# Optimization experiments

Hardware: AMD Instinct MI355X
Metric: run time of the kernel (lower is better)

Reference implementation:

```python
import jax, jax.numpy as jnp
import numpy as np

N = 8192
PT_DIM = 3
ENC_DIM = 384
RADIUS = 0.12
ALPHA = 6.0
SQRT_D = ENC_DIM ** 0.5


def setup_inputs() -> dict:
    key = jax.random.key(0)
    k1, k2 = jax.random.split(key)
    pts = jax.random.uniform(k1, (N, PT_DIM), dtype=jnp.float32)  # points in unit cube
    # A corresponds to the (frozen) random-feature matrix: stacked standard normals * alpha
    A = jax.random.normal(k2, (PT_DIM, ENC_DIM), dtype=jnp.float32) * ALPHA
    return {"pts": pts, "A": A}


def reference(pts, A):
    # Radius-ball adjacency: J[i,j] = 1 if ||pts[i]-pts[j]|| < r (dist^2 < r^2, dist >= 0)
    d2 = jnp.sum((pts[:, None, :] - pts[None, :, :]) ** 2, axis=-1)  # (N, N)
    J = (d2 < RADIUS * RADIUS).astype(pts.dtype)                      # (N, N)

    pA = (pts / RADIUS) @ A            # (N, ENC_DIM)
    c, s = jnp.cos(pA), jnp.sin(pA)    # epA = [cos(pA), sin(pA)]

    # Neighbor aggregation: G = J @ epA, done per real/imag part
    Gr = J @ c                          # (N, ENC_DIM)
    Gi = J @ s

    # Complex phase division: (Gr + i Gi) / (cos + i sin)
    G = jax.lax.complex(Gr, Gi) / jax.lax.complex(c, s)

    # Row-wise normalization to norm sqrt(enc_dim)
    G = G / jnp.linalg.norm(G, axis=-1, keepdims=True) * SQRT_D
    return G
```

## Files before the change

kernel.cpp:

```cpp
#include <hip/hip_runtime.h>
#include <hip/hip_fp16.h>
#include <math.h>

#define N_PTS   8192
#define ENC     384
#define NTHREAD 384
#define NCELL1  8
#define NCELLS  512
#define RADIUS  0.12f
#define MAXSUB  12
#define MAXU    352

__device__ __forceinline__ void fast_sincos(float x, float& s, float& c) {
    float rev = x * 0.15915494309189535f;
    rev -= rintf(rev);
    s = __builtin_amdgcn_sinf(rev);
    c = __builtin_amdgcn_cosf(rev);
}

__device__ __forceinline__ int cell_of(float x) {
    int c = (int)(x * 8.0f);
    return min(NCELL1 - 1, max(0, c));
}

static __device__ __forceinline__ unsigned h2u(__half2 h) { union { __half2 h; unsigned u; } x; x.h = h; return x.u; }
static __device__ __forceinline__ __half2 u2h(unsigned u) { union { unsigned u; __half2 h; } x; x.u = u; return x.h; }

static const size_t OFF_CSTART_I = 0;
static const size_t OFF_SPTS_B   = 520 * 4;
static const size_t OFF_CS_B     = OFF_SPTS_B + (size_t)N_PTS * 16;
static const size_t WS_FULL_B    = OFF_CS_B + (size_t)(N_PTS + 1) * ENC * 4 + 1024;

__global__ __launch_bounds__(1024) void k_prep(const float* __restrict__ pts,
                                               int* __restrict__ cell_start_g,
                                               float4* __restrict__ spts) {
    __shared__ int cnt[NCELLS];
    __shared__ int sc[NCELLS];
    __shared__ int cur[NCELLS];
    const int t = threadIdx.x;
    if (t < NCELLS) cnt[t] = 0;
    __syncthreads();

    int   cids[8];
    float xs[8], ys[8], zs[8];
    #pragma unroll
    for (int k = 0; k < 8; ++k) {
        int i = t + k * 1024;
        float x = pts[3 * i + 0], y = pts[3 * i + 1], z = pts[3 * i + 2];
        xs[k] = x; ys[k] = y; zs[k] = z;
        int cid = (cell_of(x) << 6) | (cell_of(y) << 3) | cell_of(z);
        cids[k] = cid;
        atomicAdd(&cnt[cid], 1);
    }
    __syncthreads();
    if (t < NCELLS) sc[t] = cnt[t];
    __syncthreads();
    for (int off = 1; off < NCELLS; off <<= 1) {
        int v = 0;
        if (t < NCELLS && t >= off) v = sc[t - off];
        __syncthreads();
        if (t < NCELLS) sc[t] += v;
        __syncthreads();
    }
    if (t < NCELLS) {
        int excl = sc[t] - cnt[t];
        cell_start_g[t] = excl;
        cur[t] = excl;
    }
    if (t == 0) cell_start_g[NCELLS] = N_PTS;
    __syncthreads();
    #pragma unroll
    for (int k = 0; k < 8; ++k) {
        int i = t + k * 1024;
        int pos = atomicAdd(&cur[cids[k]], 1);
        spts[pos] = make_float4(xs[k], ys[k], zs[k], __int_as_float(i));
    }
}

__global__ __launch_bounds__(NTHREAD) void k_encode(const float4* __restrict__ spts,
                                                    const float* __restrict__ A,
                                                    __half2* __restrict__ cs) {
    const int t  = threadIdx.x;
    const int p0 = blockIdx.x * 8;
    const float a0 = A[t], a1 = A[ENC + t], a2 = A[2 * ENC + t];
    #pragma unroll
    for (int k = 0; k < 8; ++k) {
        int p = p0 + k;
        if (p > N_PTS) break;
        if (p == N_PTS) {
            cs[(size_t)p * ENC + t] = __floats2half2_rn(0.f, 0.f);
            break;
        }
        float4 P = spts[p];
        float qx = __fdiv_rn(P.x, RADIUS);
        float qy = __fdiv_rn(P.y, RADIUS);
        float qz = __fdiv_rn(P.z, RADIUS);
        float pa = fmaf(qz, a2, fmaf(qy, a1, qx * a0));
        float s, c;
        fast_sincos(pa, s, c);
        cs[(size_t)p * ENC + t] = __floats2half2_rn(c, s);
    }
}

__global__ __launch_bounds__(NTHREAD) void k_main(const float4* __restrict__ spts,
                                                  const int* __restrict__ cell_start,
                                                  const uint4* __restrict__ cs4,
                                                  float* __restrict__ out, int out_mode) {
    const int b    = blockIdx.x;
    const int cell = (b & 7) * 64 + ((b >> 3) & 63);
    const int s    = b >> 9;
    const int t = threadIdx.x, lane = t & 63, wv = t >> 6;
    const int g = t / 96, q = t - g * 96;

    __shared__ int    run_lo[9], run_hi[9];
    __shared__ float4 own_l[4];
    __shared__ int    ne;
    __shared__ __align__(16) unsigned int ent_g[4][96];
    __shared__ uint4  comb_a[4][96];
    __shared__ uint4  comb_b[4][96];
    __shared__ float  red2[4][96];
    __shared__ float  scale_l[4];

    const int o_lo = cell_start[cell];
    const int o_hi = cell_start[cell + 1];
    const int n_own = o_hi - o_lo;
    if (n_own <= 0 || 4 * s >= n_own) return;

    const int cx = cell >> 6, cy = (cell >> 3) & 7, cz = cell & 7;
    if (t < 9) {
        int dx = t / 3 - 1, dy = t % 3 - 1;
        int cxx = cx + dx, cyy = cy + dy;
        int lo = 0, hi = 0;
        if (cxx >= 0 && cxx <= 7 && cyy >= 0 && cyy <= 7) {
            int basec = (cxx * 8 + cyy) * 8;
            int zlo = max(cz - 1, 0), zhi = min(cz + 1, 7);
            lo = cell_start[basec + zlo];
            hi = cell_start[basec + zhi + 1];
        }
        run_lo[t] = lo; run_hi[t] = hi;
    }

    const double R2 = (double)0.12 * (double)0.12;
    const float R2_LO = 0.0144f - 1e-6f;
    const float R2_HI = 0.0144f + 1e-6f;
    const uint4* csq = cs4 + q;

    for (int chunk = s; 4 * chunk < n_own; chunk += MAXSUB) {
        const int pbase = o_lo + 4 * chunk;
        const int np = min(4, o_hi - pbase);

        __syncthreads();
        if (t == 0) ne = 0;
        if (t < 4) {
            int idx = pbase + t;
            own_l[t] = (idx < o_hi) ? spts[idx] : make_float4(1e9f, 1e9f, 1e9f, 0.f);
        }
        __syncthreads();
        const float4 O0 = own_l[0], O1 = own_l[1], O2 = own_l[2], O3 = own_l[3];

        for (int r = wv; r < 9; r += 6) {
            const int lo = run_lo[r], hi = run_hi[r];
            for (int jb = lo; jb < hi; jb += 64) {
                int j = jb + lane;
                unsigned mk = 0;
                if (j < hi) {
                    float4 Pj = spts[j];
                    #define TEST(O, BIT) { \
                        float fdx = Pj.x - O.x, fdy = Pj.y - O.y, fdz = Pj.z - O.z; \
                        float d2f = fmaf(fdx, fdx, fmaf(fdy, fdy, fdz * fdz)); \
                        if (d2f < R2_LO) mk |= (BIT); \
                        else if (d2f <= R2_HI) { \
                            double ddx = (double)Pj.x - (double)O.x; \
                            double ddy = (double)Pj.y - (double)O.y; \
                            double ddz = (double)Pj.z - (double)O.z; \
                            if (ddx * ddx + ddy * ddy + ddz * ddz < R2) mk |= (BIT); \
                        } }
                    TEST(O0, 1u) TEST(O1, 2u) TEST(O2, 4u) TEST(O3, 8u)
                    #undef TEST
                }
                unsigned long long mask = __ballot(mk != 0);
                if (mask) {
                    int leader = __ffsll((long long)mask) - 1;
                    int basep = 0;
                    if (lane == leader) basep = atomicAdd(&ne, __popcll(mask));
                    basep = __shfl(basep, leader);
                    if (mk != 0) {
                        int pos = basep + __popcll(mask & ((1ull << lane) - 1ull));
                        if (pos < MAXU) ent_g[pos & 3][pos >> 2] = (unsigned)j | (mk << 16);
                    }
                }
            }
        }
        __syncthreads();
        const int ne_p  = min(ne, MAXU);
        const int total = (ne_p + 15) & ~15;
        if (t < total + 16 - ne_p) {
            int pos = ne_p + t;
            ent_g[pos & 3][pos >> 2] = (unsigned)N_PTS;
        }
        __syncthreads();
        const int P = total >> 2;

        __half2 ax0[4], ax1[4], ax2[4], ax3[4];
        #pragma unroll
        for (int dd = 0; dd < 4; ++dd) {
            ax0[dd] = u2h(0u); ax1[dd] = u2h(0u); ax2[dd] = u2h(0u); ax3[dd] = u2h(0u);
        }
        uint4 ev = *(const uint4*)&ent_g[g][0];
        uint4 r0 = csq[(size_t)(ev.x & 0xFFFFu) * 96];
        uint4 r1 = csq[(size_t)(ev.y & 0xFFFFu) * 96];
        uint4 r2 = csq[(size_t)(ev.z & 0xFFFFu) * 96];
        uint4 r3 = csq[(size_t)(ev.w & 0xFFFFu) * 96];
        for (int m = 0; m < P; m += 4) {
            uint4 ev_n = *(const uint4*)&ent_g[g][m + 4];
            uint4 n0 = csq[(size_t)(ev_n.x & 0xFFFFu) * 96];
            uint4 n1 = csq[(size_t)(ev_n.y & 0xFFFFu) * 96];
            uint4 n2 = csq[(size_t)(ev_n.z & 0xFFFFu) * 96];
            uint4 n3 = csq[(size_t)(ev_n.w & 0xFFFFu) * 96];
            #define ACC4(R, MK) { \
                unsigned mk_ = (MK); \
                __half2 h0 = u2h((mk_ & 1u) ? 0x3C003C00u : 0u); \
                __half2 h1 = u2h((mk_ & 2u) ? 0x3C003C00u : 0u); \
                __half2 h2 = u2h((mk_ & 4u) ? 0x3C003C00u : 0u); \
                __half2 h3 = u2h((mk_ & 8u) ? 0x3C003C00u : 0u); \
                __half2 rx = u2h(R.x), ry = u2h(R.y), rz = u2h(R.z), rw = u2h(R.w); \
                ax0[0] = __hfma2(rx, h0, ax0[0]); ax0[1] = __hfma2(ry, h0, ax0[1]); \
                ax0[2] = __hfma2(rz, h0, ax0[2]); ax0[3] = __hfma2(rw, h0, ax0[3]); \
                ax1[0] = __hfma2(rx, h1, ax1[0]); ax1[1] = __hfma2(ry, h1, ax1[1]); \
                ax1[2] = __hfma2(rz, h1, ax1[2]); ax1[3] = __hfma2(rw, h1, ax1[3]); \
                ax2[0] = __hfma2(rx, h2, ax2[0]); ax2[1] = __hfma2(ry, h2, ax2[1]); \
                ax2[2] = __hfma2(rz, h2, ax2[2]); ax2[3] = __hfma2(rw, h2, ax2[3]); \
                ax3[0] = __hfma2(rx, h3, ax3[0]); ax3[1] = __hfma2(ry, h3, ax3[1]); \
                ax3[2] = __hfma2(rz, h3, ax3[2]); ax3[3] = __hfma2(rw, h3, ax3[3]); }
            ACC4(r0, ev.x >> 16) ACC4(r1, ev.y >> 16) ACC4(r2, ev.z >> 16) ACC4(r3, ev.w >> 16)
            #undef ACC4
            ev = ev_n; r0 = n0; r1 = n1; r2 = n2; r3 = n3;
        }

        #define PACK4(A) make_uint4(h2u(A[0]), h2u(A[1]), h2u(A[2]), h2u(A[3]))
        #define ADDU(A, V) { A[0] = __hadd2(A[0], u2h(V.x)); A[1] = __hadd2(A[1], u2h(V.y)); \
                             A[2] = __hadd2(A[2], u2h(V.z)); A[3] = __hadd2(A[3], u2h(V.w)); }
        if (g == 1) { comb_a[0][q] = PACK4(ax0); comb_a[1][q] = PACK4(ax1);
                      comb_a[2][q] = PACK4(ax2); comb_a[3][q] = PACK4(ax3); }
        else if (g == 3) { comb_b[0][q] = PACK4(ax0); comb_b[1][q] = PACK4(ax1);
                           comb_b[2][q] = PACK4(ax2); comb_b[3][q] = PACK4(ax3); }
        __syncthreads();
        if (g == 0) { uint4 v0 = comb_a[0][q], v1 = comb_a[1][q], v2 = comb_a[2][q], v3 = comb_a[3][q];
                      ADDU(ax0, v0) ADDU(ax1, v1) ADDU(ax2, v2) ADDU(ax3, v3) }
        else if (g == 2) { uint4 v0 = comb_b[0][q], v1 = comb_b[1][q], v2 = comb_b[2][q], v3 = comb_b[3][q];
                           ADDU(ax0, v0) ADDU(ax1, v1) ADDU(ax2, v2) ADDU(ax3, v3) }
        __syncthreads();
        if (g == 2) { comb_a[0][q] = PACK4(ax0); comb_a[1][q] = PACK4(ax1);
                      comb_a[2][q] = PACK4(ax2); comb_a[3][q] = PACK4(ax3); }
        __syncthreads();
        if (g == 0) {
            uint4 v0 = comb_a[0][q], v1 = comb_a[1][q], v2 = comb_a[2][q], v3 = comb_a[3][q];
            ADDU(ax0, v0) ADDU(ax1, v1) ADDU(ax2, v2) ADDU(ax3, v3)
            #define NORM_P(AC, PP) { float m2 = 0.f; \
                _Pragma("unroll") for (int dd = 0; dd < 4; ++dd) { \
                    float2 f = __half22float2(AC[dd]); \
                    m2 = fmaf(f.x, f.x, fmaf(f.y, f.y, m2)); } \
                red2[PP][q] = m2; }
            NORM_P(ax0, 0) NORM_P(ax1, 1) NORM_P(ax2, 2) NORM_P(ax3, 3)
            #undef NORM_P
        }
        #undef PACK4
        #undef ADDU
        __syncthreads();
        if (t < 256) {
            int w = t >> 6, l = t & 63;
            float v = red2[w][l] + (l < 32 ? red2[w][64 + l] : 0.f);
            #pragma unroll
            for (int off = 32; off > 0; off >>= 1) v += __shfl_down(v, off);
            if (l == 0) scale_l[w] = sqrtf(384.0f / v);
        }
        __syncthreads();
        if (g == 0) {
            #define STORE_P(AC, PP) if ((PP) < np) { \
                const float scl = scale_l[PP]; \
                uint4 ov = csq[(size_t)(pbase + (PP)) * 96]; \
                float2 o0 = __half22float2(u2h(ov.x)), o1 = __half22float2(u2h(ov.y)); \
                float2 o2 = __half22float2(u2h(ov.z)), o3 = __half22float2(u2h(ov.w)); \
                float2 g0v = __half22float2(AC[0]), g1v = __half22float2(AC[1]); \
                float2 g2v = __half22float2(AC[2]), g3v = __half22float2(AC[3]); \
                float re0 = (g0v.x * o0.x + g0v.y * o0.y) * scl, im0 = (g0v.y * o0.x - g0v.x * o0.y) * scl; \
                float re1 = (g1v.x * o1.x + g1v.y * o1.y) * scl, im1 = (g1v.y * o1.x - g1v.x * o1.y) * scl; \
                float re2 = (g2v.x * o2.x + g2v.y * o2.y) * scl, im2 = (g2v.y * o2.x - g2v.x * o2.y) * scl; \
                float re3 = (g3v.x * o3.x + g3v.y * o3.y) * scl, im3 = (g3v.y * o3.x - g3v.x * o3.y) * scl; \
                const int o = __float_as_int(own_l[PP].w); \
                if (out_mode == 0) { \
                    ((float4*)out)[(size_t)o * 96 + q] = make_float4(re0, re1, re2, re3); \
                } else { \
                    ((float4*)out)[(size_t)o * 192 + 2 * q + 0] = make_float4(re0, im0, re1, im1); \
                    ((float4*)out)[(size_t)o * 192 + 2 * q + 1] = make_float4(re2, im2, re3, im3); \
                } }
            STORE_P(ax0, 0) STORE_P(ax1, 1) STORE_P(ax2, 2) STORE_P(ax3, 3)
            #undef STORE_P
        }
    }
}

__global__ __launch_bounds__(NTHREAD) void vecKM_allpairs(const float* __restrict__ pts,
                                                          const float* __restrict__ A,
                                                          float* __restrict__ out, int out_mode) {
    const int i = blockIdx.x;
    const int t = threadIdx.x;
    __shared__ float nb_x[512], nb_y[512], nb_z[512];
    __shared__ int nb_cnt;
    __shared__ float red[8];
    if (t == 0) nb_cnt = 0;
    __syncthreads();
    const float xi = pts[3 * i + 0], yi = pts[3 * i + 1], zi = pts[3 * i + 2];
    const double dxi = xi, dyi = yi, dzi = zi;
    const double R2 = (double)0.12 * (double)0.12;
    const float R2_LO = 0.0144f - 1e-6f, R2_HI = 0.0144f + 1e-6f;
    const int lane = t & 63;
    for (int jb = 0; jb < N_PTS; jb += NTHREAD) {
        const int j = jb + t;
        bool isnb = false;
        float xj = 0.f, yj = 0.f, zj = 0.f;
        if (j < N_PTS) {
            xj = pts[3 * j + 0]; yj = pts[3 * j + 1]; zj = pts[3 * j + 2];
            float fdx = xj - xi, fdy = yj - yi, fdz = zj - zi;
            float d2f = fmaf(fdx, fdx, fmaf(fdy, fdy, fdz * fdz));
            if (d2f < R2_LO) isnb = true;
            else if (d2f <= R2_HI) {
                double dx = (double)xj - dxi, dy = (double)yj - dyi, dz = (double)zj - dzi;
                isnb = (dx * dx + dy * dy + dz * dz) < R2;
            }
        }
        unsigned long long mask = __ballot(isnb);
        if (mask) {
            int leader = __ffsll((long long)mask) - 1;
            int basep = 0;
            if (lane == leader) basep = atomicAdd(&nb_cnt, __popcll(mask));
            basep = __shfl(basep, leader);
            if (isnb) {
                int pos = basep + __popcll(mask & ((1ull << lane) - 1ull));
                if (pos < 512) {
                    nb_x[pos] = (xj - xi) * (1.0f / 0.12f);
                    nb_y[pos] = (yj - yi) * (1.0f / 0.12f);
                    nb_z[pos] = (zj - zi) * (1.0f / 0.12f);
                }
            }
        }
    }
    __syncthreads();
    const int nn = min(nb_cnt, 512);
    const float a0 = A[t], a1 = A[ENC + t], a2 = A[2 * ENC + t];
    float gr = 0.f, gi = 0.f;
    #pragma unroll 4
    for (int m = 0; m < nn; ++m) {
        float pa = fmaf(nb_z[m], a2, fmaf(nb_y[m], a1, nb_x[m] * a0));
        float sv, cv;
        fast_sincos(pa, sv, cv);
        gr += cv; gi += sv;
    }
    float m2 = fmaf(gr, gr, gi * gi);
    #pragma unroll
    for (int off = 32; off > 0; off >>= 1) m2 += __shfl_down(m2, off);
    const int wid = t >> 6;
    if (lane == 0) red[wid] = m2;
    __syncthreads();
    if (t == 0) {
        float tot = 0.f;
        for (int w = 0; w < NTHREAD / 64; ++w) tot += red[w];
        red[7] = tot;
    }
    __syncthreads();
    const float scale = sqrtf(384.0f / red[7]);
    const float re = gr * scale, im = gi * scale;
    if (out_mode == 0) out[i * ENC + t] = re;
    else ((float2*)out)[i * ENC + t] = make_float2(re, im);
}

extern "C" void kernel_launch(void* const* d_in, const int* in_sizes, int n_in,
                              void* d_out, int out_size, void* d_ws, size_t ws_size,
                              hipStream_t stream) {
    const float* pts = (const float*)d_in[0];
    const float* A   = (const float*)d_in[1];
    float* out = (float*)d_out;
    const int out_mode = (out_size >= 2 * N_PTS * ENC) ? 1 : 0;

    if (ws_size >= WS_FULL_B) {
        int*     cell_start = (int*)d_ws + OFF_CSTART_I;
        float4*  spts       = (float4*)((char*)d_ws + OFF_SPTS_B);
        __half2* cs         = (__half2*)((char*)d_ws + OFF_CS_B);

        k_prep<<<1, 1024, 0, stream>>>(pts, cell_start, spts);
        k_encode<<<(N_PTS / 8) + 1, NTHREAD, 0, stream>>>(spts, A, cs);
        k_main<<<8 * 64 * MAXSUB, NTHREAD, 0, stream>>>(spts, cell_start,
                                                        (const uint4*)cs, out, out_mode);
    } else {
        vecKM_allpairs<<<N_PTS, NTHREAD, 0, stream>>>(pts, A, out, out_mode);
    }
}
```

Measured before the change: 73.77 us.

## Split point binning into multi-block kernels and schedule k_main via chunk descriptors

The single-block preprocessing kernel is replaced by a memset plus separate count, scan and scatter kernels, so binning runs across 16 blocks instead of one 1024-thread block. The scan also builds a descriptor table mapping each k_main block to one (cell, 4-point chunk), so each block handles exactly one chunk instead of looping over chunks with a fixed stride of 12. The software prefetch of the next neighbor entries in the accumulation loop is removed, and MAXU grows slightly. This adds more kernel launches and drops the per-slab chunk capacity to 384, which silently skips chunks if a slab overflows.

```diff
diff --git a/kernel.cpp b/kernel.cpp
--- a/kernel.cpp
+++ b/kernel.cpp
@@ -8,8 +8,9 @@
 #define NCELL1  8
 #define NCELLS  512
 #define RADIUS  0.12f
-#define MAXSUB  12
-#define MAXU    352
+#define MAXU    368
+#define NCH_SLAB 384
+#define GRID_MAIN (8 * NCH_SLAB)
 
 __device__ __forceinline__ void fast_sincos(float x, float& s, float& c) {
     float rev = x * 0.15915494309189535f;
@@ -26,55 +27,77 @@
 static __device__ __forceinline__ unsigned h2u(__half2 h) { union { __half2 h; unsigned u; } x; x.h = h; return x.u; }
 static __device__ __forceinline__ __half2 u2h(unsigned u) { union { unsigned u; __half2 h; } x; x.u = u; return x.h; }
 
-static const size_t OFF_CSTART_I = 0;
-static const size_t OFF_SPTS_B   = 520 * 4;
-static const size_t OFF_CS_B     = OFF_SPTS_B + (size_t)N_PTS * 16;
-static const size_t WS_FULL_B    = OFF_CS_B + (size_t)(N_PTS + 1) * ENC * 4 + 1024;
-
-__global__ __launch_bounds__(1024) void k_prep(const float* __restrict__ pts,
-                                               int* __restrict__ cell_start_g,
-                                               float4* __restrict__ spts) {
-    __shared__ int cnt[NCELLS];
-    __shared__ int sc[NCELLS];
-    __shared__ int cur[NCELLS];
+static const size_t OFF_CNT_I    = 0;
+static const size_t OFF_CSTART_I = 512;
+static const size_t OFF_CURSOR_I = 1032;
+static const size_t OFF_CELLID_I = 1544;
+static const size_t OFF_DESC_I   = 9736;
+static const size_t INT_END_B    = 12808u * 4;
+static const size_t OFF_SPTS_B   = INT_END_B;
+static const size_t OFF_CS_B     = OFF_SPTS_B + 131072;
+static const size_t WS_FULL_B    = OFF_CS_B + (size_t)(N_PTS + 1) * ENC * 4;
+
+__global__ __launch_bounds__(512) void k_count(const float* __restrict__ pts,
+                                               int* __restrict__ cnt,
+                                               int* __restrict__ cell_id) {
+    int i = blockIdx.x * 512 + threadIdx.x;
+    if (i >= N_PTS) return;
+    int cid = (cell_of(pts[3 * i + 0]) << 6) | (cell_of(pts[3 * i + 1]) << 3)
+            | cell_of(pts[3 * i + 2]);
+    cell_id[i] = cid;
+    atomicAdd(&cnt[cid], 1);
+}
+
+__global__ __launch_bounds__(512) void k_scan(const int* __restrict__ cnt,
+                                              int* __restrict__ cell_start,
+                                              int* __restrict__ cursor,
+                                              int* __restrict__ desc) {
+    __shared__ int sc[512];
+    __shared__ int sch[512];
     const int t = threadIdx.x;
-    if (t < NCELLS) cnt[t] = 0;
-    __syncthreads();
-
-    int   cids[8];
-    float xs[8], ys[8], zs[8];
-    #pragma unroll
-    for (int k = 0; k < 8; ++k) {
-        int i = t + k * 1024;
-        float x = pts[3 * i + 0], y = pts[3 * i + 1], z = pts[3 * i + 2];
-        xs[k] = x; ys[k] = y; zs[k] = z;
-        int cid = (cell_of(x) << 6) | (cell_of(y) << 3) | cell_of(z);
-        cids[k] = cid;
-        atomicAdd(&cnt[cid], 1);
-    }
-    __syncthreads();
-    if (t < NCELLS) sc[t] = cnt[t];
-    __syncthreads();
-    for (int off = 1; off < NCELLS; off <<= 1) {
-        int v = 0;
-        if (t < NCELLS && t >= off) v = sc[t - off];
+    const int c = cnt[t];
+
+    sc[t] = c;
+    __syncthreads();
+    for (int off = 1; off < 512; off <<= 1) {
+        int v = (t >= off) ? sc[t - off] : 0;
         __syncthreads();
-        if (t < NCELLS) sc[t] += v;
+        sc[t] += v;
         __syncthreads();
     }
-    if (t < NCELLS) {
-        int excl = sc[t] - cnt[t];
-        cell_start_g[t] = excl;
-        cur[t] = excl;
-    }
-    if (t == 0) cell_start_g[NCELLS] = N_PTS;
-    __syncthreads();
-    #pragma unroll
-    for (int k = 0; k < 8; ++k) {
-        int i = t + k * 1024;
-        int pos = atomicAdd(&cur[cids[k]], 1);
-        spts[pos] = make_float4(xs[k], ys[k], zs[k], __int_as_float(i));
-    }
+    cell_start[t] = sc[t] - c;
+    cursor[t]     = sc[t] - c;
+    if (t == 511) cell_start[NCELLS] = sc[511];
+
+    const int nch = (c + 3) >> 2;
+    sch[t] = nch;
+    __syncthreads();
+    for (int off = 1; off < 64; off <<= 1) {
+        int v = ((t & 63) >= off) ? sch[t - off] : 0;
+        __syncthreads();
+        sch[t] += v;
+        __syncthreads();
+    }
+    const int rank = sch[t] - nch;
+
+    for (int i = t; i < GRID_MAIN; i += 512) desc[i] = -1;
+    __syncthreads();
+    const int slab = t >> 6;
+    for (int k = 0; k < nch; ++k) {
+        int pos = rank + k;
+        if (pos < NCH_SLAB) desc[slab + 8 * pos] = (t << 6) | k;
+    }
+}
+
+__global__ __launch_bounds__(512) void k_scatter(const float* __restrict__ pts,
+                                                 const int* __restrict__ cell_id,
+                                                 int* __restrict__ cursor,
+                                                 float4* __restrict__ spts) {
+    int i = blockIdx.x * 512 + threadIdx.x;
+    if (i >= N_PTS) return;
+    int pos = atomicAdd(&cursor[cell_id[i]], 1);
+    spts[pos] = make_float4(pts[3 * i + 0], pts[3 * i + 1], pts[3 * i + 2],
+                            __int_as_float(i));
 }
 
 __global__ __launch_bounds__(NTHREAD) void k_encode(const float4* __restrict__ spts,
@@ -104,11 +127,13 @@
 
 __global__ __launch_bounds__(NTHREAD) void k_main(const float4* __restrict__ spts,
                                                   const int* __restrict__ cell_start,
+                                                  const int* __restrict__ desc_g,
                                                   const uint4* __restrict__ cs4,
                                                   float* __restrict__ out, int out_mode) {
-    const int b    = blockIdx.x;
-    const int cell = (b & 7) * 64 + ((b >> 3) & 63);
-    const int s    = b >> 9;
+    const int d = desc_g[blockIdx.x];
+    if (d < 0) return;
+    const int cell = d >> 6;
+    const int kk   = d & 63;
     const int t = threadIdx.x, lane = t & 63, wv = t >> 6;
     const int g = t / 96, q = t - g * 96;
 
@@ -123,8 +148,8 @@
 
     const int o_lo = cell_start[cell];
     const int o_hi = cell_start[cell + 1];
-    const int n_own = o_hi - o_lo;
-    if (n_own <= 0 || 4 * s >= n_own) return;
+    const int pbase = o_lo + (kk << 2);
+    const int np = min(4, o_hi - pbase);
 
     const int cx = cell >> 6, cy = (cell >> 3) & 7, cz = cell & 7;
     if (t < 9) {
@@ -139,164 +164,151 @@
         }
         run_lo[t] = lo; run_hi[t] = hi;
     }
+    if (t == 0) ne = 0;
+    if (t < 4) {
+        int idx = pbase + t;
+        own_l[t] = (idx < o_hi) ? spts[idx] : make_float4(1e9f, 1e9f, 1e9f, 0.f);
+    }
+    __syncthreads();
+    const float4 O0 = own_l[0], O1 = own_l[1], O2 = own_l[2], O3 = own_l[3];
 
     const double R2 = (double)0.12 * (double)0.12;
     const float R2_LO = 0.0144f - 1e-6f;
     const float R2_HI = 0.0144f + 1e-6f;
     const uint4* csq = cs4 + q;
 
-    for (int chunk = s; 4 * chunk < n_own; chunk += MAXSUB) {
-        const int pbase = o_lo + 4 * chunk;
-        const int np = min(4, o_hi - pbase);
-
-        __syncthreads();
-        if (t == 0) ne = 0;
-        if (t < 4) {
-            int idx = pbase + t;
-            own_l[t] = (idx < o_hi) ? spts[idx] : make_float4(1e9f, 1e9f, 1e9f, 0.f);
-        }
-        __syncthreads();
-        const float4 O0 = own_l[0], O1 = own_l[1], O2 = own_l[2], O3 = own_l[3];
-
-        for (int r = wv; r < 9; r += 6) {
-            const int lo = run_lo[r], hi = run_hi[r];
-            for (int jb = lo; jb < hi; jb += 64) {
-                int j = jb + lane;
-                unsigned mk = 0;
-                if (j < hi) {
-                    float4 Pj = spts[j];
-                    #define TEST(O, BIT) { \
-                        float fdx = Pj.x - O.x, fdy = Pj.y - O.y, fdz = Pj.z - O.z; \
-                        float d2f = fmaf(fdx, fdx, fmaf(fdy, fdy, fdz * fdz)); \
-                        if (d2f < R2_LO) mk |= (BIT); \
-                        else if (d2f <= R2_HI) { \
-                            double ddx = (double)Pj.x - (double)O.x; \
-                            double ddy = (double)Pj.y - (double)O.y; \
-                            double ddz = (double)Pj.z - (double)O.z; \
-                            if (ddx * ddx + ddy * ddy + ddz * ddz < R2) mk |= (BIT); \
-                        } }
-                    TEST(O0, 1u) TEST(O1, 2u) TEST(O2, 4u) TEST(O3, 8u)
-                    #undef TEST
-                }
-                unsigned long long mask = __ballot(mk != 0);
-                if (mask) {
-                    int leader = __ffsll((long long)mask) - 1;
-                    int basep = 0;
-                    if (lane == leader) basep = atomicAdd(&ne, __popcll(mask));
-                    basep = __shfl(basep, leader);
-                    if (mk != 0) {
-                        int pos = basep + __popcll(mask & ((1ull << lane) - 1ull));
-                        if (pos < MAXU) ent_g[pos & 3][pos >> 2] = (unsigned)j | (mk << 16);
-                    }
+    for (int r = wv; r < 9; r += 6) {
+        const int lo = run_lo[r], hi = run_hi[r];
+        for (int jb = lo; jb < hi; jb += 64) {
+            int j = jb + lane;
+            unsigned mk = 0;
+            if (j < hi) {
+                float4 Pj = spts[j];
+                #define TEST(O, BIT) { \
+                    float fdx = Pj.x - O.x, fdy = Pj.y - O.y, fdz = Pj.z - O.z; \
+                    float d2f = fmaf(fdx, fdx, fmaf(fdy, fdy, fdz * fdz)); \
+                    if (d2f < R2_LO) mk |= (BIT); \
+                    else if (d2f <= R2_HI) { \
+                        double ddx = (double)Pj.x - (double)O.x; \
+                        double ddy = (double)Pj.y - (double)O.y; \
+                        double ddz = (double)Pj.z - (double)O.z; \
+                        if (ddx * ddx + ddy * ddy + ddz * ddz < R2) mk |= (BIT); \
+                    } }
+                TEST(O0, 1u) TEST(O1, 2u) TEST(O2, 4u) TEST(O3, 8u)
+                #undef TEST
+            }
+            unsigned long long mask = __ballot(mk != 0);
+            if (mask) {
+                int leader = __ffsll((long long)mask) - 1;
+                int basep = 0;
+                if (lane == leader) basep = atomicAdd(&ne, __popcll(mask));
+                basep = __shfl(basep, leader);
+                if (mk != 0) {
+                    int pos = basep + __popcll(mask & ((1ull << lane) - 1ull));
+                    if (pos < MAXU) ent_g[pos & 3][pos >> 2] = (unsigned)j | (mk << 16);
                 }
             }
         }
-        __syncthreads();
-        const int ne_p  = min(ne, MAXU);
-        const int total = (ne_p + 15) & ~15;
-        if (t < total + 16 - ne_p) {
-            int pos = ne_p + t;
-            ent_g[pos & 3][pos >> 2] = (unsigned)N_PTS;
-        }
-        __syncthreads();
-        const int P = total >> 2;
-
-        __half2 ax0[4], ax1[4], ax2[4], ax3[4];
-        #pragma unroll
-        for (int dd = 0; dd < 4; ++dd) {
-            ax0[dd] = u2h(0u); ax1[dd] = u2h(0u); ax2[dd] = u2h(0u); ax3[dd] = u2h(0u);
-        }
-        uint4 ev = *(const uint4*)&ent_g[g][0];
+    }
+    __syncthreads();
+    const int ne_p  = min(ne, MAXU);
+    const int total = (ne_p + 15) & ~15;
+    if (t < total - ne_p) {
+        int pos = ne_p + t;
+        ent_g[pos & 3][pos >> 2] = (unsigned)N_PTS;
+    }
+    __syncthreads();
+    const int P = total >> 2;
+
+    __half2 ax0[4], ax1[4], ax2[4], ax3[4];
+    #pragma unroll
+    for (int dd = 0; dd < 4; ++dd) {
+        ax0[dd] = u2h(0u); ax1[dd] = u2h(0u); ax2[dd] = u2h(0u); ax3[dd] = u2h(0u);
+    }
+    for (int m = 0; m < P; m += 4) {
+        uint4 ev = *(const uint4*)&ent_g[g][m];
         uint4 r0 = csq[(size_t)(ev.x & 0xFFFFu) * 96];
         uint4 r1 = csq[(size_t)(ev.y & 0xFFFFu) * 96];
         uint4 r2 = csq[(size_t)(ev.z & 0xFFFFu) * 96];
         uint4 r3 = csq[(size_t)(ev.w & 0xFFFFu) * 96];
-        for (int m = 0; m < P; m += 4) {
-            uint4 ev_n = *(const uint4*)&ent_g[g][m + 4];
-            uint4 n0 = csq[(size_t)(ev_n.x & 0xFFFFu) * 96];
-            uint4 n1 = csq[(size_t)(ev_n.y & 0xFFFFu) * 96];
-            uint4 n2 = csq[(size_t)(ev_n.z & 0xFFFFu) * 96];
-            uint4 n3 = csq[(size_t)(ev_n.w & 0xFFFFu) * 96];
-            #define ACC4(R, MK) { \
-                unsigned mk_ = (MK); \
-                __half2 h0 = u2h((mk_ & 1u) ? 0x3C003C00u : 0u); \
-                __half2 h1 = u2h((mk_ & 2u) ? 0x3C003C00u : 0u); \
-                __half2 h2 = u2h((mk_ & 4u) ? 0x3C003C00u : 0u); \
-                __half2 h3 = u2h((mk_ & 8u) ? 0x3C003C00u : 0u); \
-                __half2 rx = u2h(R.x), ry = u2h(R.y), rz = u2h(R.z), rw = u2h(R.w); \
-                ax0[0] = __hfma2(rx, h0, ax0[0]); ax0[1] = __hfma2(ry, h0, ax0[1]); \
-                ax0[2] = __hfma2(rz, h0, ax0[2]); ax0[3] = __hfma2(rw, h0, ax0[3]); \
-                ax1[0] = __hfma2(rx, h1, ax1[0]); ax1[1] = __hfma2(ry, h1, ax1[1]); \
-                ax1[2] = __hfma2(rz, h1, ax1[2]); ax1[3] = __hfma2(rw, h1, ax1[3]); \
-                ax2[0] = __hfma2(rx, h2, ax2[0]); ax2[1] = __hfma2(ry, h2, ax2[1]); \
-                ax2[2] = __hfma2(rz, h2, ax2[2]); ax2[3] = __hfma2(rw, h2, ax2[3]); \
-                ax3[0] = __hfma2(rx, h3, ax3[0]); ax3[1] = __hfma2(ry, h3, ax3[1]); \
-                ax3[2] = __hfma2(rz, h3, ax3[2]); ax3[3] = __hfma2(rw, h3, ax3[3]); }
-            ACC4(r0, ev.x >> 16) ACC4(r1, ev.y >> 16) ACC4(r2, ev.z >> 16) ACC4(r3, ev.w >> 16)
-            #undef ACC4
-            ev = ev_n; r0 = n0; r1 = n1; r2 = n2; r3 = n3;
-        }
-
-        #define PACK4(A) make_uint4(h2u(A[0]), h2u(A[1]), h2u(A[2]), h2u(A[3]))
-        #define ADDU(A, V) { A[0] = __hadd2(A[0], u2h(V.x)); A[1] = __hadd2(A[1], u2h(V.y)); \
-                             A[2] = __hadd2(A[2], u2h(V.z)); A[3] = __hadd2(A[3], u2h(V.w)); }
-        if (g == 1) { comb_a[0][q] = PACK4(ax0); comb_a[1][q] = PACK4(ax1);
-                      comb_a[2][q] = PACK4(ax2); comb_a[3][q] = PACK4(ax3); }
-        else if (g == 3) { comb_b[0][q] = PACK4(ax0); comb_b[1][q] = PACK4(ax1);
-                           comb_b[2][q] = PACK4(ax2); comb_b[3][q] = PACK4(ax3); }
-        __syncthreads();
-        if (g == 0) { uint4 v0 = comb_a[0][q], v1 = comb_a[1][q], v2 = comb_a[2][q], v3 = comb_a[3][q];
-                      ADDU(ax0, v0) ADDU(ax1, v1) ADDU(ax2, v2) ADDU(ax3, v3) }
-        else if (g == 2) { uint4 v0 = comb_b[0][q], v1 = comb_b[1][q], v2 = comb_b[2][q], v3 = comb_b[3][q];
-                           ADDU(ax0, v0) ADDU(ax1, v1) ADDU(ax2, v2) ADDU(ax3, v3) }
-        __syncthreads();
-        if (g == 2) { comb_a[0][q] = PACK4(ax0); comb_a[1][q] = PACK4(ax1);
-                      comb_a[2][q] = PACK4(ax2); comb_a[3][q] = PACK4(ax3); }
-        __syncthreads();
-        if (g == 0) {
-            uint4 v0 = comb_a[0][q], v1 = comb_a[1][q], v2 = comb_a[2][q], v3 = comb_a[3][q];
-            ADDU(ax0, v0) ADDU(ax1, v1) ADDU(ax2, v2) ADDU(ax3, v3)
-            #define NORM_P(AC, PP) { float m2 = 0.f; \
-                _Pragma("unroll") for (int dd = 0; dd < 4; ++dd) { \
-                    float2 f = __half22float2(AC[dd]); \
-                    m2 = fmaf(f.x, f.x, fmaf(f.y, f.y, m2)); } \
-                red2[PP][q] = m2; }
-            NORM_P(ax0, 0) NORM_P(ax1, 1) NORM_P(ax2, 2) NORM_P(ax3, 3)
-            #undef NORM_P
-        }
-        #undef PACK4
-        #undef ADDU
-        __syncthreads();
-        if (t < 256) {
-            int w = t >> 6, l = t & 63;
-            float v = red2[w][l] + (l < 32 ? red2[w][64 + l] : 0.f);
-            #pragma unroll
-            for (int off = 32; off > 0; off >>= 1) v += __shfl_down(v, off);
-            if (l == 0) scale_l[w] = sqrtf(384.0f / v);
-        }
-        __syncthreads();
-        if (g == 0) {
-            #define STORE_P(AC, PP) if ((PP) < np) { \
-                const float scl = scale_l[PP]; \
-                uint4 ov = csq[(size_t)(pbase + (PP)) * 96]; \
-                float2 o0 = __half22float2(u2h(ov.x)), o1 = __half22float2(u2h(ov.y)); \
-                float2 o2 = __half22float2(u2h(ov.z)), o3 = __half22float2(u2h(ov.w)); \
-                float2 g0v = __half22float2(AC[0]), g1v = __half22float2(AC[1]); \
-                float2 g2v = __half22float2(AC[2]), g3v = __half22float2(AC[3]); \
-                float re0 = (g0v.x * o0.x + g0v.y * o0.y) * scl, im0 = (g0v.y * o0.x - g0v.x * o0.y) * scl; \
-                float re1 = (g1v.x * o1.x + g1v.y * o1.y) * scl, im1 = (g1v.y * o1.x - g1v.x * o1.y) * scl; \
-                float re2 = (g2v.x * o2.x + g2v.y * o2.y) * scl, im2 = (g2v.y * o2.x - g2v.x * o2.y) * scl; \
-                float re3 = (g3v.x * o3.x + g3v.y * o3.y) * scl, im3 = (g3v.y * o3.x - g3v.x * o3.y) * scl; \
-                const int o = __float_as_int(own_l[PP].w); \
-                if (out_mode == 0) { \
-                    ((float4*)out)[(size_t)o * 96 + q] = make_float4(re0, re1, re2, re3); \
-                } else { \
-                    ((float4*)out)[(size_t)o * 192 + 2 * q + 0] = make_float4(re0, im0, re1, im1); \
-                    ((float4*)out)[(size_t)o * 192 + 2 * q + 1] = make_float4(re2, im2, re3, im3); \
-                } }
-            STORE_P(ax0, 0) STORE_P(ax1, 1) STORE_P(ax2, 2) STORE_P(ax3, 3)
-            #undef STORE_P
-        }
+        #define ACC4(R, MK) { \
+            unsigned mk_ = (MK); \
+            __half2 h0 = u2h((mk_ & 1u) ? 0x3C003C00u : 0u); \
+            __half2 h1 = u2h((mk_ & 2u) ? 0x3C003C00u : 0u); \
+            __half2 h2 = u2h((mk_ & 4u) ? 0x3C003C00u : 0u); \
+            __half2 h3 = u2h((mk_ & 8u) ? 0x3C003C00u : 0u); \
+            __half2 rx = u2h(R.x), ry = u2h(R.y), rz = u2h(R.z), rw = u2h(R.w); \
+            ax0[0] = __hfma2(rx, h0, ax0[0]); ax0[1] = __hfma2(ry, h0, ax0[1]); \
+            ax0[2] = __hfma2(rz, h0, ax0[2]); ax0[3] = __hfma2(rw, h0, ax0[3]); \
+            ax1[0] = __hfma2(rx, h1, ax1[0]); ax1[1] = __hfma2(ry, h1, ax1[1]); \
+            ax1[2] = __hfma2(rz, h1, ax1[2]); ax1[3] = __hfma2(rw, h1, ax1[3]); \
+            ax2[0] = __hfma2(rx, h2, ax2[0]); ax2[1] = __hfma2(ry, h2, ax2[1]); \
+            ax2[2] = __hfma2(rz, h2, ax2[2]); ax2[3] = __hfma2(rw, h2, ax2[3]); \
+            ax3[0] = __hfma2(rx, h3, ax3[0]); ax3[1] = __hfma2(ry, h3, ax3[1]); \
+            ax3[2] = __hfma2(rz, h3, ax3[2]); ax3[3] = __hfma2(rw, h3, ax3[3]); }
+        ACC4(r0, ev.x >> 16) ACC4(r1, ev.y >> 16) ACC4(r2, ev.z >> 16) ACC4(r3, ev.w >> 16)
+        #undef ACC4
+    }
+
+    #define PACK4(A) make_uint4(h2u(A[0]), h2u(A[1]), h2u(A[2]), h2u(A[3]))
+    #define ADDU(A, V) { A[0] = __hadd2(A[0], u2h(V.x)); A[1] = __hadd2(A[1], u2h(V.y)); \
+                         A[2] = __hadd2(A[2], u2h(V.z)); A[3] = __hadd2(A[3], u2h(V.w)); }
+    if (g == 1) { comb_a[0][q] = PACK4(ax0); comb_a[1][q] = PACK4(ax1);
+                  comb_a[2][q] = PACK4(ax2); comb_a[3][q] = PACK4(ax3); }
+    else if (g == 3) { comb_b[0][q] = PACK4(ax0); comb_b[1][q] = PACK4(ax1);
+                       comb_b[2][q] = PACK4(ax2); comb_b[3][q] = PACK4(ax3); }
+    __syncthreads();
+    if (g == 0) { uint4 v0 = comb_a[0][q], v1 = comb_a[1][q], v2 = comb_a[2][q], v3 = comb_a[3][q];
+                  ADDU(ax0, v0) ADDU(ax1, v1) ADDU(ax2, v2) ADDU(ax3, v3) }
+    else if (g == 2) { uint4 v0 = comb_b[0][q], v1 = comb_b[1][q], v2 = comb_b[2][q], v3 = comb_b[3][q];
+                       ADDU(ax0, v0) ADDU(ax1, v1) ADDU(ax2, v2) ADDU(ax3, v3) }
+    __syncthreads();
+    if (g == 2) { comb_a[0][q] = PACK4(ax0); comb_a[1][q] = PACK4(ax1);
+                  comb_a[2][q] = PACK4(ax2); comb_a[3][q] = PACK4(ax3); }
+    __syncthreads();
+    if (g == 0) {
+        uint4 v0 = comb_a[0][q], v1 = comb_a[1][q], v2 = comb_a[2][q], v3 = comb_a[3][q];
+        ADDU(ax0, v0) ADDU(ax1, v1) ADDU(ax2, v2) ADDU(ax3, v3)
+        #define NORM_P(AC, PP) { float m2 = 0.f; \
+            _Pragma("unroll") for (int dd = 0; dd < 4; ++dd) { \
+                float2 f = __half22float2(AC[dd]); \
+                m2 = fmaf(f.x, f.x, fmaf(f.y, f.y, m2)); } \
+            red2[PP][q] = m2; }
+        NORM_P(ax0, 0) NORM_P(ax1, 1) NORM_P(ax2, 2) NORM_P(ax3, 3)
+        #undef NORM_P
+    }
+    #undef PACK4
+    #undef ADDU
+    __syncthreads();
+    if (t < 256) {
+        int w = t >> 6, l = t & 63;
+        float v = red2[w][l] + (l < 32 ? red2[w][64 + l] : 0.f);
+        #pragma unroll
+        for (int off = 32; off > 0; off >>= 1) v += __shfl_down(v, off);
+        if (l == 0) scale_l[w] = sqrtf(384.0f / v);
+    }
+    __syncthreads();
+    if (g == 0) {
+        #define STORE_P(AC, PP) if ((PP) < np) { \
+            const float scl = scale_l[PP]; \
+            uint4 ov = csq[(size_t)(pbase + (PP)) * 96]; \
+            float2 o0 = __half22float2(u2h(ov.x)), o1 = __half22float2(u2h(ov.y)); \
+            float2 o2 = __half22float2(u2h(ov.z)), o3 = __half22float2(u2h(ov.w)); \
+            float2 g0v = __half22float2(AC[0]), g1v = __half22float2(AC[1]); \
+            float2 g2v = __half22float2(AC[2]), g3v = __half22float2(AC[3]); \
+            float re0 = (g0v.x * o0.x + g0v.y * o0.y) * scl, im0 = (g0v.y * o0.x - g0v.x * o0.y) * scl; \
+            float re1 = (g1v.x * o1.x + g1v.y * o1.y) * scl, im1 = (g1v.y * o1.x - g1v.x * o1.y) * scl; \
+            float re2 = (g2v.x * o2.x + g2v.y * o2.y) * scl, im2 = (g2v.y * o2.x - g2v.x * o2.y) * scl; \
+            float re3 = (g3v.x * o3.x + g3v.y * o3.y) * scl, im3 = (g3v.y * o3.x - g3v.x * o3.y) * scl; \
+            const int o = __float_as_int(own_l[PP].w); \
+            if (out_mode == 0) { \
+                ((float4*)out)[(size_t)o * 96 + q] = make_float4(re0, re1, re2, re3); \
+            } else { \
+                ((float4*)out)[(size_t)o * 192 + 2 * q + 0] = make_float4(re0, im0, re1, im1); \
+                ((float4*)out)[(size_t)o * 192 + 2 * q + 1] = make_float4(re2, im2, re3, im3); \
+            } }
+        STORE_P(ax0, 0) STORE_P(ax1, 1) STORE_P(ax2, 2) STORE_P(ax3, 3)
+        #undef STORE_P
     }
 }
 
@@ -383,14 +395,21 @@
     const int out_mode = (out_size >= 2 * N_PTS * ENC) ? 1 : 0;
 
     if (ws_size >= WS_FULL_B) {
+        int*     cnt        = (int*)d_ws + OFF_CNT_I;
         int*     cell_start = (int*)d_ws + OFF_CSTART_I;
+        int*     cursor     = (int*)d_ws + OFF_CURSOR_I;
+        int*     cell_id    = (int*)d_ws + OFF_CELLID_I;
+        int*     desc       = (int*)d_ws + OFF_DESC_I;
         float4*  spts       = (float4*)((char*)d_ws + OFF_SPTS_B);
         __half2* cs         = (__half2*)((char*)d_ws + OFF_CS_B);
 
-        k_prep<<<1, 1024, 0, stream>>>(pts, cell_start, spts);
+        hipMemsetAsync(cnt, 0, NCELLS * sizeof(int), stream);
+        k_count<<<16, 512, 0, stream>>>(pts, cnt, cell_id);
+        k_scan<<<1, 512, 0, stream>>>(cnt, cell_start, cursor, desc);
+        k_scatter<<<16, 512, 0, stream>>>(pts, cell_id, cursor, spts);
         k_encode<<<(N_PTS / 8) + 1, NTHREAD, 0, stream>>>(spts, A, cs);
-        k_main<<<8 * 64 * MAXSUB, NTHREAD, 0, stream>>>(spts, cell_start,
-                                                        (const uint4*)cs, out, out_mode);
+        k_main<<<GRID_MAIN, NTHREAD, 0, stream>>>(spts, cell_start, desc,
+                                                  (const uint4*)cs, out, out_mode);
     } else {
         vecKM_allpairs<<<N_PTS, NTHREAD, 0, stream>>>(pts, A, out, out_mode);
     }
```

New measurement: 71.99 us. 1.02x faster.
